# Performance work log

Hardware: AMD Instinct MI355X
Metric: run time of the kernel (lower is better)

Reference implementation:

```python
import math
import jax, jax.numpy as jnp
import numpy as np

BITS = 8
MSE_BITS = BITS - 1          # TurboQuantProd uses bits-1 for the MSE stage
BLOCK = 128                  # block_size == dim == 128 -> no padding path
EPS = 1e-10

# ---- Lloyd-Max codebook for unit Gaussian (computed once in numpy) ----
_erf = np.vectorize(math.erf)

def _pdf(t):
    t = np.clip(t, -30.0, 30.0)
    return np.exp(-0.5 * t * t) / np.sqrt(2.0 * np.pi)

def _cdf(t):
    t = np.clip(t, -30.0, 30.0)
    return 0.5 * (1.0 + _erf(t / np.sqrt(2.0)))

def _lloyd_max_codebook(bits, iters=200):
    L = 2 ** bits
    lv = np.linspace(-4.0, 4.0, L)
    for _ in range(iters):
        b = 0.5 * (lv[:-1] + lv[1:])
        lo = np.concatenate([[-30.0], b])
        hi = np.concatenate([b, [30.0]])
        lv = (_pdf(lo) - _pdf(hi)) / np.maximum(_cdf(hi) - _cdf(lo), 1e-30)
    return lv.astype(np.float32)

CODEBOOK = _lloyd_max_codebook(MSE_BITS)                 # [128] levels
BOUNDS = 0.5 * (CODEBOOK[:-1] + CODEBOOK[1:])            # [127] decision boundaries

# ---- normalized fast Walsh-Hadamard transform (orthonormal -> self-inverse) ----
def fwht(x):
    n = x.shape[-1]
    shp = x.shape
    y = x.reshape(-1, n)
    h = 1
    while h < n:
        y = y.reshape(-1, n // (2 * h), 2, h)
        y = jnp.stack([y[:, :, 0, :] + y[:, :, 1, :], y[:, :, 0, :] - y[:, :, 1, :]], axis=2)
        y = y.reshape(-1, n)
        h *= 2
    return (y * np.float32(1.0 / np.sqrt(n))).reshape(shp)

def rotation_fwd(x, rot_signs):
    # cascaded SRHT: per pass, sign flip then Hadamard
    for p in range(rot_signs.shape[0]):
        x = fwht(x * rot_signs[p])
    return x

def rotation_inv(x, rot_signs):
    for p in range(rot_signs.shape[0] - 1, -1, -1):
        x = fwht(x) * rot_signs[p]
    return x

def lm_quantize(x):
    return jnp.searchsorted(jnp.asarray(BOUNDS, x.dtype), x)

def lm_dequantize(idx, dtype):
    return jnp.asarray(CODEBOOK, dtype)[idx]


def setup_inputs() -> dict:
    key = jax.random.key(0)
    k1, k2, k3 = jax.random.split(key, 3)
    x = jax.random.normal(k1, (2, 32, 4096, 128), dtype=jnp.float32)
    rot_signs = jnp.where(jax.random.uniform(k2, (2, 128)) < 0.5, -1.0, 1.0).astype(jnp.float32)
    qjl_signs = jnp.where(jax.random.uniform(k3, (128,)) < 0.5, -1.0, 1.0).astype(jnp.float32)
    return {"x": x, "rot_signs": rot_signs, "qjl_signs": qjl_signs}


def reference(x, rot_signs, qjl_signs):
    # ===== TurboQuantProd.quantize =====
    norms = jnp.linalg.norm(x, axis=-1)                                  # [...]
    x_unit = x / (norms[..., None] + EPS)
    x_rot = rotation_fwd(x_unit, rot_signs)                              # [..., 128]
    # first-pass RMS scale + Lloyd-Max, then inner-product-refined gamma
    rms = jnp.linalg.norm(x_rot, axis=-1, keepdims=True) * np.float32(1.0 / np.sqrt(BLOCK))
    recon_tmp = lm_dequantize(lm_quantize(x_rot / (rms + EPS)), x.dtype)
    num = jnp.sum(x_rot * recon_tmp, axis=-1, keepdims=True)
    den = jnp.sum(recon_tmp * recon_tmp, axis=-1, keepdims=True) + EPS
    gamma = num / den                                                    # refined scale
    idx = lm_quantize(x_rot / (gamma + EPS))                             # MSE-stage indices
    recon_unit = lm_dequantize(idx, x.dtype)
    recon_rot = recon_unit * gamma
    residual = x_rot - recon_rot                                         # rotated-domain residual
    # QJL 1-bit sketch of residual: sign flip + Hadamard, keep sign bits
    res_proj = fwht(residual * qjl_signs)
    sign_bits = (res_proj >= 0)
    res_norms = jnp.linalg.norm(residual, axis=-1) * norms
    # ===== TurboQuantProd.dequantize =====
    signs_f = sign_bits.astype(x.dtype) * 2.0 - 1.0
    direction = fwht(signs_f) * qjl_signs                                # ifwht == fwht (orthonormal)
    dir_norm = jnp.linalg.norm(direction, axis=-1, keepdims=True) + EPS
    unit_res = res_norms / (norms + EPS)
    res_est = direction * (unit_res[..., None] / dir_norm)
    combined = recon_rot + res_est
    x_back = rotation_inv(combined, rot_signs)
    return x_back * norms[..., None]
```

## Files before the change

### kernel.cpp

```cpp
#include <hip/hip_runtime.h>
#include <math.h>

#pragma clang fp contract(off)

#define EPSF 1e-10f
#define INV128 0.0078125f
#define C128 0.08838834764831845f

struct CbArg { float cb[128]; };

template<int CTRL>
__device__ __forceinline__ float fdpp(float v) {
    return __builtin_bit_cast(float,
        __builtin_amdgcn_update_dpp(0, __builtin_bit_cast(int, v), CTRL, 0xF, 0xF, true));
}
__device__ __forceinline__ float dpp_xor4(float v) {
    const int x = __builtin_bit_cast(int, v);
    int t = __builtin_amdgcn_update_dpp(x, x, 0x124, 0xF, 0x5, false);
    t = __builtin_amdgcn_update_dpp(t, x, 0x12C, 0xF, 0xA, false);
    return __builtin_bit_cast(float, t);
}
template<int MODE, int D>
__device__ __forceinline__ float xl(float v) {
    if constexpr (MODE == 0)   return __shfl_xor(v, D, 64);
    else if constexpr (D == 1) return fdpp<0xB1>(v);
    else if constexpr (D == 2) return fdpp<0x4E>(v);
    else                       return dpp_xor4(v);
}

__device__ __forceinline__ bool dpp_ok() {
    const int lane = threadIdx.x & 63;
    const float tv = __int_as_float(0x3f800000 + lane * 1024);
    bool ok = true;
    ok = ok && (__float_as_uint(xl<1,1>(tv)) == __float_as_uint(__shfl_xor(tv, 1, 64)));
    ok = ok && (__float_as_uint(xl<1,2>(tv)) == __float_as_uint(__shfl_xor(tv, 2, 64)));
    ok = ok && (__float_as_uint(xl<1,4>(tv)) == __float_as_uint(__shfl_xor(tv, 4, 64)));
    return __all((int)ok) != 0;
}

__device__ __forceinline__ float lm_recon(const float4* __restrict__ tbl4, float v) {
    float cf = fminf(fmaxf(fmaf(v, 128.0f, 512.0f), 0.0f), 1023.0f);
    const float4 e = tbl4[(int)cf];
    return (e.x < v) ? e.z : e.y;
}

template<int MODE>
__device__ __forceinline__ void fwht_in(float* u) {
#pragma unroll
    for (int d = 1; d <= 8; d <<= 1)
#pragma unroll
        for (int j = 0; j < 16; ++j)
            if ((j & d) == 0) {
                const float a = u[j], b = u[j + d];
                u[j] = a + b; u[j + d] = a - b;
            }
}

template<int MODE>
__device__ __forceinline__ void fwht128g(float* u, float s1, float s2, float s4) {
    fwht_in<MODE>(u);
#pragma unroll
    for (int j = 0; j < 16; ++j) { const float p = xl<MODE,1>(u[j]); u[j] = fmaf(s1, u[j], p); }
#pragma unroll
    for (int j = 0; j < 16; ++j) { const float p = xl<MODE,2>(u[j]); u[j] = fmaf(s2, u[j], p); }
#pragma unroll
    for (int j = 0; j < 16; ++j) { const float p = xl<MODE,4>(u[j]); u[j] = fmaf(s4, u[j], p); }
}

template<int MODE>
__device__ __forceinline__ float rtree(const float* q) {
    float t8[8];
#pragma unroll
    for (int k = 0; k < 8; ++k) t8[k] = q[2 * k] + q[2 * k + 1];
    float t4[4];
#pragma unroll
    for (int k = 0; k < 4; ++k) t4[k] = t8[2 * k] + t8[2 * k + 1];
    const float t2a = t4[0] + t4[1];
    const float t2b = t4[2] + t4[3];
    float s = t2a + t2b;
    s += xl<MODE, 1>(s);
    s += xl<MODE, 2>(s);
    s += xl<MODE, 4>(s);
    return s;
}

template<int MODE>
__device__ __forceinline__ void run_groups(
        const float* __restrict__ x, float* __restrict__ out,
        const float* __restrict__ rot, const float* __restrict__ qjl,
        const float4* __restrict__ tbl4, int nrows) {
    const int t    = threadIdx.x;
    const int lane = t & 63;
    const int wid  = t >> 6;
    const int sub  = lane & 7;
    const int grp  = lane >> 3;

    const float s1 = (sub & 1) ? -1.0f : 1.0f;
    const float s2 = (sub & 2) ? -1.0f : 1.0f;
    const float s4 = (sub & 4) ? -1.0f : 1.0f;

    const int ngroups = nrows >> 3;
    const int gstride = gridDim.x * 4;

    for (int g0 = blockIdx.x * 4 + wid; g0 < ngroups; g0 += gstride) {
        const int row  = g0 * 8 + grp;
        const int lrow = (row < nrows) ? row : (nrows - 1);
        const float* xp = x + (size_t)lrow * 128 + sub * 16;

        float u[16], q[16], c0[16];
#pragma unroll
        for (int k = 0; k < 4; ++k) {
            const float4 v4 = ((const float4*)xp)[k];
            u[4 * k] = v4.x; u[4 * k + 1] = v4.y; u[4 * k + 2] = v4.z; u[4 * k + 3] = v4.w;
        }

#pragma unroll
        for (int j = 0; j < 16; ++j) q[j] = u[j] * u[j];
        const float nu = sqrtf(rtree<MODE>(q));
        const float iu = 1.0f / (nu + EPSF);

#pragma unroll
        for (int k = 0; k < 4; ++k) {
            const float4 v4 = ((const float4*)(rot + sub * 16))[k];
            c0[4 * k] = v4.x; c0[4 * k + 1] = v4.y; c0[4 * k + 2] = v4.z; c0[4 * k + 3] = v4.w;
        }
#pragma unroll
        for (int j = 0; j < 16; ++j) { u[j] = u[j] * iu; u[j] = u[j] * c0[j]; }

        fwht128g<MODE>(u, s1, s2, s4);
#pragma unroll
        for (int j = 0; j < 16; ++j) u[j] *= C128;
#pragma unroll
        for (int k = 0; k < 4; ++k) {
            const float4 v4 = ((const float4*)(rot + 128 + sub * 16))[k];
            c0[4 * k] = v4.x; c0[4 * k + 1] = v4.y; c0[4 * k + 2] = v4.z; c0[4 * k + 3] = v4.w;
        }
#pragma unroll
        for (int j = 0; j < 16; ++j) u[j] *= c0[j];
        fwht128g<MODE>(u, s1, s2, s4);
#pragma unroll
        for (int j = 0; j < 16; ++j) u[j] *= C128;

#pragma unroll
        for (int j = 0; j < 16; ++j) q[j] = u[j] * u[j];
        const float rms = sqrtf(rtree<MODE>(q)) * C128;
        const float si  = 1.0f / (rms + EPSF);
        float r[16];
#pragma unroll
        for (int j = 0; j < 16; ++j) r[j] = lm_recon(tbl4, u[j] * si);

#pragma unroll
        for (int j = 0; j < 16; ++j) q[j] = u[j] * r[j];
        const float num = rtree<MODE>(q);
#pragma unroll
        for (int j = 0; j < 16; ++j) q[j] = r[j] * r[j];
        const float den = rtree<MODE>(q);
        const float gamma = num / (den + EPSF);
        const float gi    = 1.0f / (gamma + EPSF);

        float rc[16], p[16];
#pragma unroll
        for (int j = 0; j < 16; ++j) {
            const float tq = lm_recon(tbl4, u[j] * gi);
            rc[j] = tq * gamma;
            p[j]  = u[j] - rc[j];
        }
#pragma unroll
        for (int j = 0; j < 16; ++j) q[j] = p[j] * p[j];
        const float resn = sqrtf(rtree<MODE>(q));

#pragma unroll
        for (int k = 0; k < 4; ++k) {
            const float4 v4 = ((const float4*)(qjl + sub * 16))[k];
            c0[4 * k] = v4.x; c0[4 * k + 1] = v4.y; c0[4 * k + 2] = v4.z; c0[4 * k + 3] = v4.w;
        }
#pragma unroll
        for (int j = 0; j < 16; ++j) p[j] = p[j] * c0[j];
        fwht128g<MODE>(p, s1, s2, s4);
#pragma unroll
        for (int j = 0; j < 16; ++j) p[j] = (p[j] >= 0.0f) ? 1.0f : -1.0f;
        fwht128g<MODE>(p, s1, s2, s4);
        const float rsc = resn * INV128;
#pragma unroll
        for (int j = 0; j < 16; ++j) {
            const float tq = p[j] * c0[j];
            p[j] = fmaf(tq, rsc, rc[j]);
        }

        fwht128g<MODE>(p, s1, s2, s4);
#pragma unroll
        for (int k = 0; k < 4; ++k) {
            const float4 v4 = ((const float4*)(rot + 128 + sub * 16))[k];
            c0[4 * k] = v4.x; c0[4 * k + 1] = v4.y; c0[4 * k + 2] = v4.z; c0[4 * k + 3] = v4.w;
        }
#pragma unroll
        for (int j = 0; j < 16; ++j) p[j] *= c0[j];
        fwht128g<MODE>(p, s1, s2, s4);
#pragma unroll
        for (int k = 0; k < 4; ++k) {
            const float4 v4 = ((const float4*)(rot + sub * 16))[k];
            c0[4 * k] = v4.x; c0[4 * k + 1] = v4.y; c0[4 * k + 2] = v4.z; c0[4 * k + 3] = v4.w;
        }
        const float fn = nu * INV128;
#pragma unroll
        for (int j = 0; j < 16; ++j) p[j] = (p[j] * c0[j]) * fn;

        if (row < nrows) {
            float* op = out + (size_t)row * 128 + sub * 16;
#pragma unroll
            for (int k = 0; k < 4; ++k) {
                float4 v4;
                v4.x = p[4 * k]; v4.y = p[4 * k + 1]; v4.z = p[4 * k + 2]; v4.w = p[4 * k + 3];
                ((float4*)op)[k] = v4;
            }
        }
    }
}

__global__ __launch_bounds__(256) void turboquant_kernel(
        const float* __restrict__ x,
        const float* __restrict__ rot,
        const float* __restrict__ qjl,
        float* __restrict__ out,
        const int nrows,
        const CbArg args) {
    __shared__ float scb[128];
    __shared__ float sbnd[128];
    __shared__ float4 tbl4[1024];

    const int t = threadIdx.x;
    if (t < 128) scb[t] = args.cb[t];
    __syncthreads();
    if (t < 128) {
        const float INF = __int_as_float(0x7f800000);
        sbnd[t] = (t < 127) ? 0.5f * (scb[t] + scb[t + 1]) : INF;
    }
    __syncthreads();
    for (int c = t; c < 1024; c += 256) {
        const float cl = -4.0f + (float)c * 0.0078125f;
        int g = 0;
#pragma unroll
        for (int d = 64; d >= 1; d >>= 1) g += (sbnd[g + d - 1] < cl) ? d : 0;
        tbl4[c] = make_float4(sbnd[g], scb[g], scb[(g < 127) ? g + 1 : 127], 0.0f);
    }
    __syncthreads();

    if (dpp_ok())
        run_groups<1>(x, out, rot, qjl, tbl4, nrows);
    else
        run_groups<0>(x, out, rot, qjl, tbl4, nrows);
}

static void lloyd_host(CbArg* out_args) {
    double lv[128], bp[127], bc[127];
    for (int i = 0; i < 128; ++i)
        lv[i] = (i == 127) ? 4.0 : (-4.0 + (8.0 / 127.0) * (double)i);

    const double inv_sqrt2pi = 0.39894228040143267794;
    const double inv_sqrt2   = 0.70710678118654752440;
    const double pdf_end = exp(-0.5 * 30.0 * 30.0) * inv_sqrt2pi;
    const double cdf_m30 = 0.5 * (1.0 + erf(-30.0 * inv_sqrt2));
    const double cdf_p30 = 0.5 * (1.0 + erf( 30.0 * inv_sqrt2));

    for (int it = 0; it < 200; ++it) {
        for (int i = 0; i < 127; ++i) {
            double tt = 0.5 * (lv[i] + lv[i + 1]);
            tt = fmin(fmax(tt, -30.0), 30.0);
            bp[i] = exp(-0.5 * tt * tt) * inv_sqrt2pi;
            bc[i] = 0.5 * (1.0 + erf(tt * inv_sqrt2));
        }
        for (int i = 0; i < 128; ++i) {
            const double plo = (i == 0)   ? pdf_end : bp[i - 1];
            const double clo = (i == 0)   ? cdf_m30 : bc[i - 1];
            const double phi = (i == 127) ? pdf_end : bp[i];
            const double chi = (i == 127) ? cdf_p30 : bc[i];
            lv[i] = (plo - phi) / fmax(chi - clo, 1e-30);
        }
    }
    for (int i = 0; i < 128; ++i) out_args->cb[i] = (float)lv[i];
}

extern "C" void kernel_launch(void* const* d_in, const int* in_sizes, int n_in,
                              void* d_out, int out_size, void* d_ws, size_t ws_size,
                              hipStream_t stream) {
    const float* x   = (const float*)d_in[0];
    const float* rot = (const float*)d_in[1];
    const float* qjl = (const float*)d_in[2];
    float* out = (float*)d_out;
    (void)d_ws; (void)ws_size;

    const int nrows = in_sizes[0] >> 7;

    CbArg args;
    lloyd_host(&args);

    turboquant_kernel<<<2048, 256, 0, stream>>>(x, rot, qjl, out, nrows, args);
}
```

Measured before the change: 150.0 us.

## Split each 128-wide row across 16 lanes instead of 8

Each row is now processed by 16 lanes holding 8 elements each, so a wavefront handles 4 rows instead of 8. The FWHT and reductions gain an extra cross-lane butterfly stage, done with a row_ror:8 DPP (0x128) that is checked against shfl_xor at startup. This halves per-thread registers and in-thread butterfly work, which should raise occupancy and parallelism, at the cost of more cross-lane DPP ops per element and more loop iterations. The partial-group row clamp and bounds check were removed, so the code now assumes the row count is a multiple of 4.

```diff
diff --git a/kernel.cpp b/kernel.cpp
--- a/kernel.cpp
+++ b/kernel.cpp
@@ -25,7 +25,8 @@
     if constexpr (MODE == 0)   return __shfl_xor(v, D, 64);
     else if constexpr (D == 1) return fdpp<0xB1>(v);
     else if constexpr (D == 2) return fdpp<0x4E>(v);
-    else                       return dpp_xor4(v);
+    else if constexpr (D == 4) return dpp_xor4(v);
+    else                       return fdpp<0x128>(v);
 }
 
 __device__ __forceinline__ bool dpp_ok() {
@@ -35,6 +36,7 @@
     ok = ok && (__float_as_uint(xl<1,1>(tv)) == __float_as_uint(__shfl_xor(tv, 1, 64)));
     ok = ok && (__float_as_uint(xl<1,2>(tv)) == __float_as_uint(__shfl_xor(tv, 2, 64)));
     ok = ok && (__float_as_uint(xl<1,4>(tv)) == __float_as_uint(__shfl_xor(tv, 4, 64)));
+    ok = ok && (__float_as_uint(xl<1,8>(tv)) == __float_as_uint(__shfl_xor(tv, 8, 64)));
     return __all((int)ok) != 0;
 }
 
@@ -44,12 +46,11 @@
     return (e.x < v) ? e.z : e.y;
 }
 
-template<int MODE>
-__device__ __forceinline__ void fwht_in(float* u) {
-#pragma unroll
-    for (int d = 1; d <= 8; d <<= 1)
-#pragma unroll
-        for (int j = 0; j < 16; ++j)
+__device__ __forceinline__ void fwht_in8(float* u) {
+#pragma unroll
+    for (int d = 1; d <= 4; d <<= 1)
+#pragma unroll
+        for (int j = 0; j < 8; ++j)
             if ((j & d) == 0) {
                 const float a = u[j], b = u[j + d];
                 u[j] = a + b; u[j + d] = a - b;
@@ -57,30 +58,30 @@
 }
 
 template<int MODE>
-__device__ __forceinline__ void fwht128g(float* u, float s1, float s2, float s4) {
-    fwht_in<MODE>(u);
-#pragma unroll
-    for (int j = 0; j < 16; ++j) { const float p = xl<MODE,1>(u[j]); u[j] = fmaf(s1, u[j], p); }
-#pragma unroll
-    for (int j = 0; j < 16; ++j) { const float p = xl<MODE,2>(u[j]); u[j] = fmaf(s2, u[j], p); }
-#pragma unroll
-    for (int j = 0; j < 16; ++j) { const float p = xl<MODE,4>(u[j]); u[j] = fmaf(s4, u[j], p); }
+__device__ __forceinline__ void fwht128g(float* u, float s1, float s2, float s4, float s8) {
+    fwht_in8(u);
+#pragma unroll
+    for (int j = 0; j < 8; ++j) { const float p = xl<MODE,1>(u[j]); u[j] = fmaf(s1, u[j], p); }
+#pragma unroll
+    for (int j = 0; j < 8; ++j) { const float p = xl<MODE,2>(u[j]); u[j] = fmaf(s2, u[j], p); }
+#pragma unroll
+    for (int j = 0; j < 8; ++j) { const float p = xl<MODE,4>(u[j]); u[j] = fmaf(s4, u[j], p); }
+#pragma unroll
+    for (int j = 0; j < 8; ++j) { const float p = xl<MODE,8>(u[j]); u[j] = fmaf(s8, u[j], p); }
 }
 
 template<int MODE>
 __device__ __forceinline__ float rtree(const float* q) {
-    float t8[8];
-#pragma unroll
-    for (int k = 0; k < 8; ++k) t8[k] = q[2 * k] + q[2 * k + 1];
     float t4[4];
 #pragma unroll
-    for (int k = 0; k < 4; ++k) t4[k] = t8[2 * k] + t8[2 * k + 1];
+    for (int k = 0; k < 4; ++k) t4[k] = q[2 * k] + q[2 * k + 1];
     const float t2a = t4[0] + t4[1];
     const float t2b = t4[2] + t4[3];
     float s = t2a + t2b;
     s += xl<MODE, 1>(s);
     s += xl<MODE, 2>(s);
     s += xl<MODE, 4>(s);
+    s += xl<MODE, 8>(s);
     return s;
 }
 
@@ -92,127 +93,125 @@
     const int t    = threadIdx.x;
     const int lane = t & 63;
     const int wid  = t >> 6;
-    const int sub  = lane & 7;
-    const int grp  = lane >> 3;
+    const int sub  = lane & 15;
+    const int grp  = lane >> 4;
 
     const float s1 = (sub & 1) ? -1.0f : 1.0f;
     const float s2 = (sub & 2) ? -1.0f : 1.0f;
     const float s4 = (sub & 4) ? -1.0f : 1.0f;
-
-    const int ngroups = nrows >> 3;
+    const float s8 = (sub & 8) ? -1.0f : 1.0f;
+
+    const int ngroups = nrows >> 2;
     const int gstride = gridDim.x * 4;
 
     for (int g0 = blockIdx.x * 4 + wid; g0 < ngroups; g0 += gstride) {
-        const int row  = g0 * 8 + grp;
-        const int lrow = (row < nrows) ? row : (nrows - 1);
-        const float* xp = x + (size_t)lrow * 128 + sub * 16;
-
-        float u[16], q[16], c0[16];
-#pragma unroll
-        for (int k = 0; k < 4; ++k) {
+        const int row = g0 * 4 + grp;
+        const float* xp = x + (size_t)row * 128 + sub * 8;
+
+        float u[8], q[8], c0[8];
+#pragma unroll
+        for (int k = 0; k < 2; ++k) {
             const float4 v4 = ((const float4*)xp)[k];
             u[4 * k] = v4.x; u[4 * k + 1] = v4.y; u[4 * k + 2] = v4.z; u[4 * k + 3] = v4.w;
         }
 
 #pragma unroll
-        for (int j = 0; j < 16; ++j) q[j] = u[j] * u[j];
+        for (int j = 0; j < 8; ++j) q[j] = u[j] * u[j];
         const float nu = sqrtf(rtree<MODE>(q));
         const float iu = 1.0f / (nu + EPSF);
 
 #pragma unroll
-        for (int k = 0; k < 4; ++k) {
-            const float4 v4 = ((const float4*)(rot + sub * 16))[k];
-            c0[4 * k] = v4.x; c0[4 * k + 1] = v4.y; c0[4 * k + 2] = v4.z; c0[4 * k + 3] = v4.w;
-        }
-#pragma unroll
-        for (int j = 0; j < 16; ++j) { u[j] = u[j] * iu; u[j] = u[j] * c0[j]; }
-
-        fwht128g<MODE>(u, s1, s2, s4);
-#pragma unroll
-        for (int j = 0; j < 16; ++j) u[j] *= C128;
-#pragma unroll
-        for (int k = 0; k < 4; ++k) {
-            const float4 v4 = ((const float4*)(rot + 128 + sub * 16))[k];
-            c0[4 * k] = v4.x; c0[4 * k + 1] = v4.y; c0[4 * k + 2] = v4.z; c0[4 * k + 3] = v4.w;
-        }
-#pragma unroll
-        for (int j = 0; j < 16; ++j) u[j] *= c0[j];
-        fwht128g<MODE>(u, s1, s2, s4);
-#pragma unroll
-        for (int j = 0; j < 16; ++j) u[j] *= C128;
-
-#pragma unroll
-        for (int j = 0; j < 16; ++j) q[j] = u[j] * u[j];
+        for (int k = 0; k < 2; ++k) {
+            const float4 v4 = ((const float4*)(rot + sub * 8))[k];
+            c0[4 * k] = v4.x; c0[4 * k + 1] = v4.y; c0[4 * k + 2] = v4.z; c0[4 * k + 3] = v4.w;
+        }
+#pragma unroll
+        for (int j = 0; j < 8; ++j) { u[j] = u[j] * iu; u[j] = u[j] * c0[j]; }
+
+        fwht128g<MODE>(u, s1, s2, s4, s8);
+#pragma unroll
+        for (int j = 0; j < 8; ++j) u[j] *= C128;
+#pragma unroll
+        for (int k = 0; k < 2; ++k) {
+            const float4 v4 = ((const float4*)(rot + 128 + sub * 8))[k];
+            c0[4 * k] = v4.x; c0[4 * k + 1] = v4.y; c0[4 * k + 2] = v4.z; c0[4 * k + 3] = v4.w;
+        }
+#pragma unroll
+        for (int j = 0; j < 8; ++j) u[j] *= c0[j];
+        fwht128g<MODE>(u, s1, s2, s4, s8);
+#pragma unroll
+        for (int j = 0; j < 8; ++j) u[j] *= C128;
+
+#pragma unroll
+        for (int j = 0; j < 8; ++j) q[j] = u[j] * u[j];
         const float rms = sqrtf(rtree<MODE>(q)) * C128;
         const float si  = 1.0f / (rms + EPSF);
-        float r[16];
-#pragma unroll
-        for (int j = 0; j < 16; ++j) r[j] = lm_recon(tbl4, u[j] * si);
-
-#pragma unroll
-        for (int j = 0; j < 16; ++j) q[j] = u[j] * r[j];
+        float r[8];
+#pragma unroll
+        for (int j = 0; j < 8; ++j) r[j] = lm_recon(tbl4, u[j] * si);
+
+#pragma unroll
+        for (int j = 0; j < 8; ++j) q[j] = u[j] * r[j];
         const float num = rtree<MODE>(q);
 #pragma unroll
-        for (int j = 0; j < 16; ++j) q[j] = r[j] * r[j];
+        for (int j = 0; j < 8; ++j) q[j] = r[j] * r[j];
         const float den = rtree<MODE>(q);
         const float gamma = num / (den + EPSF);
         const float gi    = 1.0f / (gamma + EPSF);
 
-        float rc[16], p[16];
-#pragma unroll
-        for (int j = 0; j < 16; ++j) {
+        float rc[8], p[8];
+#pragma unroll
+        for (int j = 0; j < 8; ++j) {
             const float tq = lm_recon(tbl4, u[j] * gi);
             rc[j] = tq * gamma;
             p[j]  = u[j] - rc[j];
         }
 #pragma unroll
-        for (int j = 0; j < 16; ++j) q[j] = p[j] * p[j];
+        for (int j = 0; j < 8; ++j) q[j] = p[j] * p[j];
         const float resn = sqrtf(rtree<MODE>(q));
 
 #pragma unroll
-        for (int k = 0; k < 4; ++k) {
-            const float4 v4 = ((const float4*)(qjl + sub * 16))[k];
-            c0[4 * k] = v4.x; c0[4 * k + 1] = v4.y; c0[4 * k + 2] = v4.z; c0[4 * k + 3] = v4.w;
-        }
-#pragma unroll
-        for (int j = 0; j < 16; ++j) p[j] = p[j] * c0[j];
-        fwht128g<MODE>(p, s1, s2, s4);
-#pragma unroll
-        for (int j = 0; j < 16; ++j) p[j] = (p[j] >= 0.0f) ? 1.0f : -1.0f;
-        fwht128g<MODE>(p, s1, s2, s4);
+        for (int k = 0; k < 2; ++k) {
+            const float4 v4 = ((const float4*)(qjl + sub * 8))[k];
+            c0[4 * k] = v4.x; c0[4 * k + 1] = v4.y; c0[4 * k + 2] = v4.z; c0[4 * k + 3] = v4.w;
+        }
+#pragma unroll
+        for (int j = 0; j < 8; ++j) p[j] = p[j] * c0[j];
+        fwht128g<MODE>(p, s1, s2, s4, s8);
+#pragma unroll
+        for (int j = 0; j < 8; ++j) p[j] = (p[j] >= 0.0f) ? 1.0f : -1.0f;
+        fwht128g<MODE>(p, s1, s2, s4, s8);
         const float rsc = resn * INV128;
 #pragma unroll
-        for (int j = 0; j < 16; ++j) {
+        for (int j = 0; j < 8; ++j) {
             const float tq = p[j] * c0[j];
             p[j] = fmaf(tq, rsc, rc[j]);
         }
 
-        fwht128g<MODE>(p, s1, s2, s4);
-#pragma unroll
-        for (int k = 0; k < 4; ++k) {
-            const float4 v4 = ((const float4*)(rot + 128 + sub * 16))[k];
-            c0[4 * k] = v4.x; c0[4 * k + 1] = v4.y; c0[4 * k + 2] = v4.z; c0[4 * k + 3] = v4.w;
-        }
-#pragma unroll
-        for (int j = 0; j < 16; ++j) p[j] *= c0[j];
-        fwht128g<MODE>(p, s1, s2, s4);
-#pragma unroll
-        for (int k = 0; k < 4; ++k) {
-            const float4 v4 = ((const float4*)(rot + sub * 16))[k];
+        fwht128g<MODE>(p, s1, s2, s4, s8);
+#pragma unroll
+        for (int k = 0; k < 2; ++k) {
+            const float4 v4 = ((const float4*)(rot + 128 + sub * 8))[k];
+            c0[4 * k] = v4.x; c0[4 * k + 1] = v4.y; c0[4 * k + 2] = v4.z; c0[4 * k + 3] = v4.w;
+        }
+#pragma unroll
+        for (int j = 0; j < 8; ++j) p[j] *= c0[j];
+        fwht128g<MODE>(p, s1, s2, s4, s8);
+#pragma unroll
+        for (int k = 0; k < 2; ++k) {
+            const float4 v4 = ((const float4*)(rot + sub * 8))[k];
             c0[4 * k] = v4.x; c0[4 * k + 1] = v4.y; c0[4 * k + 2] = v4.z; c0[4 * k + 3] = v4.w;
         }
         const float fn = nu * INV128;
 #pragma unroll
-        for (int j = 0; j < 16; ++j) p[j] = (p[j] * c0[j]) * fn;
-
-        if (row < nrows) {
-            float* op = out + (size_t)row * 128 + sub * 16;
-#pragma unroll
-            for (int k = 0; k < 4; ++k) {
-                float4 v4;
-                v4.x = p[4 * k]; v4.y = p[4 * k + 1]; v4.z = p[4 * k + 2]; v4.w = p[4 * k + 3];
-                ((float4*)op)[k] = v4;
-            }
+        for (int j = 0; j < 8; ++j) p[j] = (p[j] * c0[j]) * fn;
+
+        float* op = out + (size_t)row * 128 + sub * 8;
+#pragma unroll
+        for (int k = 0; k < 2; ++k) {
+            float4 v4;
+            v4.x = p[4 * k]; v4.y = p[4 * k + 1]; v4.z = p[4 * k + 2]; v4.w = p[4 * k + 3];
+            ((float4*)op)[k] = v4;
         }
     }
 }
```

New measurement: 184.7 us. +23.1%, slower.

## Prefetch next row group into registers and stage sign vectors in LDS

Applied to the files above, without the earlier changes.

Software-pipelines the grid-stride loop by loading the next group's input row into registers while the current group is computed, so global-load latency overlaps with the long transform chain. The rotation and QJL sign vectors are copied into shared memory once per block instead of being re-read from global memory in every iteration. The row<nrows guard is dropped, which assumes nrows is a multiple of 8. The prefetch costs 16 extra registers per thread, which may reduce occupancy.

```diff
diff --git a/kernel.cpp b/kernel.cpp
--- a/kernel.cpp
+++ b/kernel.cpp
@@ -44,8 +44,7 @@
     return (e.x < v) ? e.z : e.y;
 }
 
-template<int MODE>
-__device__ __forceinline__ void fwht_in(float* u) {
+__device__ __forceinline__ void fwht_in16(float* u) {
 #pragma unroll
     for (int d = 1; d <= 8; d <<= 1)
 #pragma unroll
@@ -58,7 +57,7 @@
 
 template<int MODE>
 __device__ __forceinline__ void fwht128g(float* u, float s1, float s2, float s4) {
-    fwht_in<MODE>(u);
+    fwht_in16(u);
 #pragma unroll
     for (int j = 0; j < 16; ++j) { const float p = xl<MODE,1>(u[j]); u[j] = fmaf(s1, u[j], p); }
 #pragma unroll
@@ -87,7 +86,7 @@
 template<int MODE>
 __device__ __forceinline__ void run_groups(
         const float* __restrict__ x, float* __restrict__ out,
-        const float* __restrict__ rot, const float* __restrict__ qjl,
+        const float* __restrict__ srot, const float* __restrict__ sqj,
         const float4* __restrict__ tbl4, int nrows) {
     const int t    = threadIdx.x;
     const int lane = t & 63;
@@ -101,18 +100,36 @@
 
     const int ngroups = nrows >> 3;
     const int gstride = gridDim.x * 4;
-
-    for (int g0 = blockIdx.x * 4 + wid; g0 < ngroups; g0 += gstride) {
-        const int row  = g0 * 8 + grp;
-        const int lrow = (row < nrows) ? row : (nrows - 1);
-        const float* xp = x + (size_t)lrow * 128 + sub * 16;
-
+    const int g0start = blockIdx.x * 4 + wid;
+    if (g0start >= ngroups) return;
+
+    float xu[16];
+    {
+        const float* xp = x + (size_t)(g0start * 8 + grp) * 128 + sub * 16;
+#pragma unroll
+        for (int k = 0; k < 4; ++k) {
+            const float4 v4 = ((const float4*)xp)[k];
+            xu[4*k] = v4.x; xu[4*k+1] = v4.y; xu[4*k+2] = v4.z; xu[4*k+3] = v4.w;
+        }
+    }
+
+    for (int g0 = g0start; g0 < ngroups; g0 += gstride) {
+        float xn[16];
+        {
+            const int g1   = g0 + gstride;
+            const int prow = ((g1 < ngroups) ? g1 : g0) * 8 + grp;
+            const float* xp = x + (size_t)prow * 128 + sub * 16;
+#pragma unroll
+            for (int k = 0; k < 4; ++k) {
+                const float4 v4 = ((const float4*)xp)[k];
+                xn[4*k] = v4.x; xn[4*k+1] = v4.y; xn[4*k+2] = v4.z; xn[4*k+3] = v4.w;
+            }
+        }
+
+        const int row = g0 * 8 + grp;
         float u[16], q[16], c0[16];
 #pragma unroll
-        for (int k = 0; k < 4; ++k) {
-            const float4 v4 = ((const float4*)xp)[k];
-            u[4 * k] = v4.x; u[4 * k + 1] = v4.y; u[4 * k + 2] = v4.z; u[4 * k + 3] = v4.w;
-        }
+        for (int j = 0; j < 16; ++j) u[j] = xu[j];
 
 #pragma unroll
         for (int j = 0; j < 16; ++j) q[j] = u[j] * u[j];
@@ -121,8 +138,8 @@
 
 #pragma unroll
         for (int k = 0; k < 4; ++k) {
-            const float4 v4 = ((const float4*)(rot + sub * 16))[k];
-            c0[4 * k] = v4.x; c0[4 * k + 1] = v4.y; c0[4 * k + 2] = v4.z; c0[4 * k + 3] = v4.w;
+            const float4 v4 = ((const float4*)(srot + sub * 16))[k];
+            c0[4*k] = v4.x; c0[4*k+1] = v4.y; c0[4*k+2] = v4.z; c0[4*k+3] = v4.w;
         }
 #pragma unroll
         for (int j = 0; j < 16; ++j) { u[j] = u[j] * iu; u[j] = u[j] * c0[j]; }
@@ -132,8 +149,8 @@
         for (int j = 0; j < 16; ++j) u[j] *= C128;
 #pragma unroll
         for (int k = 0; k < 4; ++k) {
-            const float4 v4 = ((const float4*)(rot + 128 + sub * 16))[k];
-            c0[4 * k] = v4.x; c0[4 * k + 1] = v4.y; c0[4 * k + 2] = v4.z; c0[4 * k + 3] = v4.w;
+            const float4 v4 = ((const float4*)(srot + 128 + sub * 16))[k];
+            c0[4*k] = v4.x; c0[4*k+1] = v4.y; c0[4*k+2] = v4.z; c0[4*k+3] = v4.w;
         }
 #pragma unroll
         for (int j = 0; j < 16; ++j) u[j] *= c0[j];
@@ -171,8 +188,8 @@
 
 #pragma unroll
         for (int k = 0; k < 4; ++k) {
-            const float4 v4 = ((const float4*)(qjl + sub * 16))[k];
-            c0[4 * k] = v4.x; c0[4 * k + 1] = v4.y; c0[4 * k + 2] = v4.z; c0[4 * k + 3] = v4.w;
+            const float4 v4 = ((const float4*)(sqj + sub * 16))[k];
+            c0[4*k] = v4.x; c0[4*k+1] = v4.y; c0[4*k+2] = v4.z; c0[4*k+3] = v4.w;
         }
 #pragma unroll
         for (int j = 0; j < 16; ++j) p[j] = p[j] * c0[j];
@@ -190,30 +207,31 @@
         fwht128g<MODE>(p, s1, s2, s4);
 #pragma unroll
         for (int k = 0; k < 4; ++k) {
-            const float4 v4 = ((const float4*)(rot + 128 + sub * 16))[k];
-            c0[4 * k] = v4.x; c0[4 * k + 1] = v4.y; c0[4 * k + 2] = v4.z; c0[4 * k + 3] = v4.w;
+            const float4 v4 = ((const float4*)(srot + 128 + sub * 16))[k];
+            c0[4*k] = v4.x; c0[4*k+1] = v4.y; c0[4*k+2] = v4.z; c0[4*k+3] = v4.w;
         }
 #pragma unroll
         for (int j = 0; j < 16; ++j) p[j] *= c0[j];
         fwht128g<MODE>(p, s1, s2, s4);
 #pragma unroll
         for (int k = 0; k < 4; ++k) {
-            const float4 v4 = ((const float4*)(rot + sub * 16))[k];
-            c0[4 * k] = v4.x; c0[4 * k + 1] = v4.y; c0[4 * k + 2] = v4.z; c0[4 * k + 3] = v4.w;
+            const float4 v4 = ((const float4*)(srot + sub * 16))[k];
+            c0[4*k] = v4.x; c0[4*k+1] = v4.y; c0[4*k+2] = v4.z; c0[4*k+3] = v4.w;
         }
         const float fn = nu * INV128;
 #pragma unroll
         for (int j = 0; j < 16; ++j) p[j] = (p[j] * c0[j]) * fn;
 
-        if (row < nrows) {
-            float* op = out + (size_t)row * 128 + sub * 16;
-#pragma unroll
-            for (int k = 0; k < 4; ++k) {
-                float4 v4;
-                v4.x = p[4 * k]; v4.y = p[4 * k + 1]; v4.z = p[4 * k + 2]; v4.w = p[4 * k + 3];
-                ((float4*)op)[k] = v4;
-            }
-        }
+        float* op = out + (size_t)row * 128 + sub * 16;
+#pragma unroll
+        for (int k = 0; k < 4; ++k) {
+            float4 v4;
+            v4.x = p[4*k]; v4.y = p[4*k+1]; v4.z = p[4*k+2]; v4.w = p[4*k+3];
+            ((float4*)op)[k] = v4;
+        }
+
+#pragma unroll
+        for (int j = 0; j < 16; ++j) xu[j] = xn[j];
     }
 }
 
@@ -227,9 +245,16 @@
     __shared__ float scb[128];
     __shared__ float sbnd[128];
     __shared__ float4 tbl4[1024];
+    __shared__ float srot[256];
+    __shared__ float sqj[128];
 
     const int t = threadIdx.x;
-    if (t < 128) scb[t] = args.cb[t];
+    if (t < 128) {
+        scb[t]  = args.cb[t];
+        srot[t] = rot[t];
+        srot[128 + t] = rot[128 + t];
+        sqj[t]  = qjl[t];
+    }
     __syncthreads();
     if (t < 128) {
         const float INF = __int_as_float(0x7f800000);
@@ -246,9 +271,9 @@
     __syncthreads();
 
     if (dpp_ok())
-        run_groups<1>(x, out, rot, qjl, tbl4, nrows);
+        run_groups<1>(x, out, srot, sqj, tbl4, nrows);
     else
-        run_groups<0>(x, out, rot, qjl, tbl4, nrows);
+        run_groups<0>(x, out, srot, sqj, tbl4, nrows);
 }
 
 static void lloyd_host(CbArg* out_args) {
```

After: 158.9 us. +5.9%, slower.
